# Kernel tuning notes

Measured on AMD Instinct MI355X. Metric: run time of the kernel, lower is better.

## Reference

```python
import jax, jax.numpy as jnp
import numpy as np

D_MODEL = 1024
H = 16
D_K = D_MODEL // H  # 64
B, S = 2, 2048


def setup_inputs() -> dict:
    key = jax.random.key(0)
    ks = jax.random.split(key, 8)
    scale = 1.0 / np.sqrt(D_MODEL)
    return {
        "q": jax.random.normal(ks[0], (B, S, D_MODEL), dtype=jnp.float32),
        "k": jax.random.normal(ks[1], (B, S, D_MODEL), dtype=jnp.float32),
        "v": jax.random.normal(ks[2], (B, S, D_MODEL), dtype=jnp.float32),
        "W_q": jax.random.normal(ks[3], (H, D_MODEL, D_K), dtype=jnp.float32) * scale,
        "W_k": jax.random.normal(ks[4], (H, D_MODEL, D_K), dtype=jnp.float32) * scale,
        "W_v": jax.random.normal(ks[5], (H, D_MODEL, D_K), dtype=jnp.float32) * scale,
        "W_o": jax.random.normal(ks[6], (D_MODEL, H * D_K), dtype=jnp.float32) * scale,
        "b_o": jnp.zeros((D_MODEL,), dtype=jnp.float32),
    }


def reference(q, k, v, W_q, W_k, W_v, W_o, b_o):
    b, s, _ = q.shape
    h, _, d_k = W_q.shape
    inv_sqrt_dk = jnp.asarray(1.0 / np.sqrt(d_k), q.dtype)
    # per-head projections: [b, h, s, d_k]
    qh = jnp.einsum("bsd,hdk->bhsk", q, W_q)
    kh = jnp.einsum("bsd,hdk->bhsk", k, W_k)
    vh = jnp.einsum("bsd,hdk->bhsk", v, W_v)
    # scaled dot product attention
    scores = jnp.einsum("bhqk,bhsk->bhqs", qh, kh) * inv_sqrt_dk  # [b,h,S,S]
    attn = jax.nn.softmax(scores, axis=-1)
    ctx = jnp.einsum("bhqs,bhsk->bhqk", attn, vh)  # [b,h,S,d_k]
    # chunk over heads + concat along feature dim -> [b, S, h*d_k], head-major
    ctx = ctx.transpose(0, 2, 1, 3).reshape(b, s, h * d_k)
    # final linear
    return ctx @ W_o.T + b_o
```

## Files before the change

### kernel.cpp

```cpp
#include <hip/hip_runtime.h>
#include <cstdint>
#include <cstddef>


typedef unsigned short bf16_t;
typedef __attribute__((ext_vector_type(8))) short short8;
typedef __attribute__((ext_vector_type(4))) float f32x4;

#define GLB_AS(p) ((const __attribute__((address_space(1))) void*)(p))
#define LDS_AS(p) ((__attribute__((address_space(3))) void*)(p))

__device__ __forceinline__ uint32_t fbits(float f) {
  union { float f; uint32_t u; } v; v.f = f; return v.u;
}
__device__ __forceinline__ bf16_t f2bf(float f) {
  uint32_t u = fbits(f);
  return (bf16_t)((u + 0x7FFFu + ((u >> 16) & 1u)) >> 16);
}
__device__ __forceinline__ uint32_t packbf2(float lo, float hi) {
  uint32_t a = fbits(hi) + 0x8000u;
  uint32_t b = fbits(lo) + 0x8000u;
  return __builtin_amdgcn_perm(a, b, 0x07060302u);
}

__global__ void prep_kernel(const float* __restrict__ q, const float* __restrict__ k,
                            const float* __restrict__ v, const float* __restrict__ Wo,
                            const float* __restrict__ Wq, const float* __restrict__ Wk,
                            const float* __restrict__ Wv,
                            bf16_t* __restrict__ qo, bf16_t* __restrict__ ko,
                            bf16_t* __restrict__ vo, bf16_t* __restrict__ Woo,
                            bf16_t* __restrict__ Wtq, bf16_t* __restrict__ Wtk,
                            bf16_t* __restrict__ Wtv) {
  int blk = blockIdx.x;
  int tid = threadIdx.x;
  if (blk < 13312) {
    const float* src; bf16_t* dst; int i;
    if (blk < 4096)       { src = q;  dst = qo;  i = blk * 256 + tid; }
    else if (blk < 8192)  { src = k;  dst = ko;  i = (blk - 4096) * 256 + tid; }
    else if (blk < 12288) { src = v;  dst = vo;  i = (blk - 8192) * 256 + tid; }
    else                  { src = Wo; dst = Woo; i = (blk - 12288) * 256 + tid; }
    f32x4 val = ((const f32x4*)src)[i];
    ushort4 o;
    o.x = f2bf(val.x); o.y = f2bf(val.y); o.z = f2bf(val.z); o.w = f2bf(val.w);
    ((ushort4*)dst)[i] = o;
  } else {
    int blk2 = blk - 13312;
    int z = blk2 >> 9, t = blk2 & 511;
    const float* W = z == 0 ? Wq : z == 1 ? Wk : Wv;
    bf16_t* Wt = z == 0 ? Wtq : z == 1 ? Wtk : Wtv;
    int h = t >> 5, d0 = (t & 31) * 32;
    __shared__ float tile[32][65];
    const float* src = W + ((size_t)h << 16) + (size_t)d0 * 64;
    int d = tid >> 3;
#pragma unroll
    for (int j = 0; j < 2; j++) {
      int dk = (tid & 7) * 8 + j * 4;
      *(f32x4*)&tile[d][dk] = *(const f32x4*)(src + d * 64 + dk);
    }
    __syncthreads();
    int dk2 = tid >> 2, c = tid & 3;
    union { ushort s[8]; int4 v; } o;
#pragma unroll
    for (int j = 0; j < 8; j++) o.s[j] = f2bf(tile[c * 8 + j][dk2]);
    *(int4*)(Wt + (size_t)(h * 64 + dk2) * 1024 + d0 + c * 8) = o.v;
  }
}

__global__ void v_transpose_kernel(const bf16_t* __restrict__ vh, bf16_t* __restrict__ vT) {
  __shared__ bf16_t tile[64][72];
  const int tid = threadIdx.x;
  const int s0 = blockIdx.x * 64;
  const size_t bh = blockIdx.y;
  const bf16_t* src = vh + bh * (2048 * 64) + (size_t)s0 * 64;
#pragma unroll
  for (int j = 0; j < 2; j++) {
    int cidx = tid + j * 256, s = cidx >> 3, ck = cidx & 7;
    *(int4*)(&tile[s][ck * 8]) = *(const int4*)(src + s * 64 + ck * 8);
  }
  __syncthreads();
  bf16_t* dst = vT + bh * (64 * 2048) + s0;
#pragma unroll
  for (int j = 0; j < 2; j++) {
    int cidx = tid + j * 256, dk = cidx >> 3, cs = cidx & 7;
    union { ushort s[8]; int4 v; } o;
#pragma unroll
    for (int e = 0; e < 8; e++) o.s[e] = tile[cs * 8 + e][dk];
    *(int4*)(dst + (size_t)dk * 2048 + cs * 8) = o.v;
  }
}

__global__ __launch_bounds__(256) void gemm_proj_kernel(
    const bf16_t* __restrict__ A0, const bf16_t* __restrict__ A1, const bf16_t* __restrict__ A2,
    const bf16_t* __restrict__ B0, const bf16_t* __restrict__ B1, const bf16_t* __restrict__ B2,
    bf16_t* __restrict__ O0, bf16_t* __restrict__ O1, bf16_t* __restrict__ O2,
    float s0)
{
  const int z = blockIdx.z;
  const bf16_t* A  = z == 0 ? A0 : z == 1 ? A1 : A2;
  const bf16_t* Bt = z == 0 ? B0 : z == 1 ? B1 : B2;
  bf16_t* Cbf      = z == 0 ? O0 : z == 1 ? O1 : O2;
  const float scale = z == 0 ? s0 : 1.0f;
  const int K = 1024;

  __shared__ alignas(16) bf16_t Asmem[128 * 32];
  __shared__ alignas(16) bf16_t Bsmem[128 * 32];
  const int tid = threadIdx.x;
  const int lane = tid & 63, wave = tid >> 6;
  const int wm = wave >> 1, wn = wave & 1;
  const int quad = lane >> 4, l15 = lane & 15;
  const int m0 = blockIdx.y * 128, n0 = blockIdx.x * 128;

  f32x4 acc[4][4];
#pragma unroll
  for (int i = 0; i < 4; i++)
#pragma unroll
    for (int j = 0; j < 4; j++) acc[i][j] = (f32x4)0.0f;

  const int c0 = wave * 128 + lane;
  const int c1 = wave * 128 + 64 + lane;

  for (int k0 = 0; k0 < K; k0 += 32) {
    __builtin_amdgcn_global_load_lds(GLB_AS(A  + (size_t)(m0 + (c0 >> 2)) * K + k0 + (c0 & 3) * 8),
                                     LDS_AS(Asmem + c0 * 8), 16, 0, 0);
    __builtin_amdgcn_global_load_lds(GLB_AS(A  + (size_t)(m0 + (c1 >> 2)) * K + k0 + (c1 & 3) * 8),
                                     LDS_AS(Asmem + c1 * 8), 16, 0, 0);
    __builtin_amdgcn_global_load_lds(GLB_AS(Bt + (size_t)(n0 + (c0 >> 2)) * K + k0 + (c0 & 3) * 8),
                                     LDS_AS(Bsmem + c0 * 8), 16, 0, 0);
    __builtin_amdgcn_global_load_lds(GLB_AS(Bt + (size_t)(n0 + (c1 >> 2)) * K + k0 + (c1 & 3) * 8),
                                     LDS_AS(Bsmem + c1 * 8), 16, 0, 0);
    __syncthreads();

    short8 af[4], bfr[4];
#pragma unroll
    for (int mi = 0; mi < 4; mi++)
      af[mi] = *(const short8*)(Asmem + (wm * 64 + mi * 16 + l15) * 32 + quad * 8);
#pragma unroll
    for (int ni = 0; ni < 4; ni++)
      bfr[ni] = *(const short8*)(Bsmem + (wn * 64 + ni * 16 + l15) * 32 + quad * 8);
#pragma unroll
    for (int mi = 0; mi < 4; mi++)
#pragma unroll
      for (int ni = 0; ni < 4; ni++)
        acc[mi][ni] = __builtin_amdgcn_mfma_f32_16x16x32_bf16(af[mi], bfr[ni], acc[mi][ni], 0, 0, 0);
    __syncthreads();
  }

#pragma unroll
  for (int ni = 0; ni < 4; ni++) {
    int col = n0 + wn * 64 + ni * 16 + l15;
    int h = col >> 6, dk = col & 63;
#pragma unroll
    for (int mi = 0; mi < 4; mi++) {
      int row = m0 + wm * 64 + mi * 16 + quad * 4;
#pragma unroll
      for (int r = 0; r < 4; r++) {
        int g = row + r;
        int b = g >> 11, s = g & 2047;
        Cbf[((size_t)((b * 16 + h) * 2048 + s)) * 64 + dk] = f2bf(acc[mi][ni][r] * scale);
      }
    }
  }
}

__global__ __launch_bounds__(256) void gemm_out_kernel(
    const bf16_t* __restrict__ A, const bf16_t* __restrict__ Bt,
    float* __restrict__ C, const float* __restrict__ bias)
{
  const int K = 1024, N = 1024;
  __shared__ alignas(16) bf16_t Asmem[128 * 32];
  __shared__ alignas(16) bf16_t Bsmem[64 * 32];
  const int tid = threadIdx.x;
  const int lane = tid & 63, wave = tid >> 6;
  const int quad = lane >> 4, l15 = lane & 15;
  const int m0 = blockIdx.y * 128, n0 = blockIdx.x * 64;

  f32x4 acc[2][4];
#pragma unroll
  for (int i = 0; i < 2; i++)
#pragma unroll
    for (int j = 0; j < 4; j++) acc[i][j] = (f32x4)0.0f;

  const int c0 = wave * 128 + lane;
  const int c1 = wave * 128 + 64 + lane;
  const int cb = wave * 64 + lane;

  for (int k0 = 0; k0 < K; k0 += 32) {
    __builtin_amdgcn_global_load_lds(GLB_AS(A  + (size_t)(m0 + (c0 >> 2)) * K + k0 + (c0 & 3) * 8),
                                     LDS_AS(Asmem + c0 * 8), 16, 0, 0);
    __builtin_amdgcn_global_load_lds(GLB_AS(A  + (size_t)(m0 + (c1 >> 2)) * K + k0 + (c1 & 3) * 8),
                                     LDS_AS(Asmem + c1 * 8), 16, 0, 0);
    __builtin_amdgcn_global_load_lds(GLB_AS(Bt + (size_t)(n0 + (cb >> 2)) * K + k0 + (cb & 3) * 8),
                                     LDS_AS(Bsmem + cb * 8), 16, 0, 0);
    __syncthreads();

    short8 af[2], bfr[4];
#pragma unroll
    for (int mi = 0; mi < 2; mi++)
      af[mi] = *(const short8*)(Asmem + (wave * 32 + mi * 16 + l15) * 32 + quad * 8);
#pragma unroll
    for (int ni = 0; ni < 4; ni++)
      bfr[ni] = *(const short8*)(Bsmem + (ni * 16 + l15) * 32 + quad * 8);
#pragma unroll
    for (int mi = 0; mi < 2; mi++)
#pragma unroll
      for (int ni = 0; ni < 4; ni++)
        acc[mi][ni] = __builtin_amdgcn_mfma_f32_16x16x32_bf16(af[mi], bfr[ni], acc[mi][ni], 0, 0, 0);
    __syncthreads();
  }

#pragma unroll
  for (int ni = 0; ni < 4; ni++) {
    int col = n0 + ni * 16 + l15;
    float bv = bias[col];
#pragma unroll
    for (int mi = 0; mi < 2; mi++) {
      int row = m0 + wave * 32 + mi * 16 + quad * 4;
#pragma unroll
      for (int r = 0; r < 4; r++)
        C[(size_t)(row + r) * N + col] = acc[mi][ni][r] + bv;
    }
  }
}

__global__ __launch_bounds__(512) void flash_kernel(
    const bf16_t* __restrict__ qh, const bf16_t* __restrict__ kh,
    const bf16_t* __restrict__ vT, bf16_t* __restrict__ ctx)
{
  __shared__ alignas(16) bf16_t Kt[2][64 * 72];
  __shared__ alignas(16) bf16_t Vt[2][64 * 72];
  __shared__ alignas(16) bf16_t Pt[8][16 * 72];
  const int tid = threadIdx.x, lane = tid & 63, wave = tid >> 6;
  const int quad = lane >> 4, l15 = lane & 15;
  const int q0 = blockIdx.x * 128;
  const int h = blockIdx.y, b = blockIdx.z;
  const size_t headoff = (size_t)(b * 16 + h) * 2048 * 64;
  const bf16_t* Q = qh + headoff;
  const bf16_t* K = kh + headoff;
  const bf16_t* V = vT + headoff;
  bf16_t* Ptw = &Pt[wave][0];

  const int qrow = q0 + wave * 16 + l15;
  short8 qf[2];
#pragma unroll
  for (int ks = 0; ks < 2; ks++)
    qf[ks] = *(const short8*)(Q + (size_t)qrow * 64 + ks * 32 + quad * 8);

  f32x4 O[4];
#pragma unroll
  for (int mi = 0; mi < 4; mi++) O[mi] = (f32x4)0.0f;
  f32x4 lacc = (f32x4)0.0f;

  const int sr = tid >> 3, scc = tid & 7;
  const bf16_t* Kp = K + (size_t)sr * 64 + scc * 8;
  const bf16_t* Vp = V + (size_t)sr * 2048 + scc * 8;
  const int soff = sr * 72 + scc * 8;

  int4 kreg = *(const int4*)Kp;
  int4 vreg = *(const int4*)Vp;
  *(int4*)(&Kt[0][soff]) = kreg;
  *(int4*)(&Vt[0][soff]) = vreg;
  __syncthreads();

  for (int it = 0; it < 32; ++it) {
    const int cur = it & 1, nxt = cur ^ 1;
    if (it < 31) {
      kreg = *(const int4*)(Kp + (size_t)(it + 1) * 64 * 64);
      vreg = *(const int4*)(Vp + (it + 1) * 64);
    }

    f32x4 S[4];
#pragma unroll
    for (int mi = 0; mi < 4; mi++) S[mi] = (f32x4)0.0f;
#pragma unroll
    for (int ks = 0; ks < 2; ks++) {
#pragma unroll
      for (int mi = 0; mi < 4; mi++) {
        short8 kf = *(const short8*)(&Kt[cur][(mi * 16 + l15) * 72 + ks * 32 + quad * 8]);
        S[mi] = __builtin_amdgcn_mfma_f32_16x16x32_bf16(kf, qf[ks], S[mi], 0, 0, 0);
      }
    }

#pragma unroll
    for (int mi = 0; mi < 4; mi++)
#pragma unroll
      for (int r = 0; r < 4; r++)
        S[mi][r] = __builtin_amdgcn_exp2f(S[mi][r]);
    lacc += (S[0] + S[1]) + (S[2] + S[3]);

#pragma unroll
    for (int mi = 0; mi < 4; mi++) {
      uint2 pk = make_uint2(packbf2(S[mi][0], S[mi][1]), packbf2(S[mi][2], S[mi][3]));
      *(uint2*)(Ptw + l15 * 72 + mi * 16 + quad * 4) = pk;
    }

#pragma unroll
    for (int ks = 0; ks < 2; ks++) {
      short8 pfrag = *(const short8*)(Ptw + l15 * 72 + ks * 32 + quad * 8);
#pragma unroll
      for (int mi = 0; mi < 4; mi++) {
        short8 vf = *(const short8*)(&Vt[cur][(mi * 16 + l15) * 72 + ks * 32 + quad * 8]);
        O[mi] = __builtin_amdgcn_mfma_f32_16x16x32_bf16(vf, pfrag, O[mi], 0, 0, 0);
      }
    }

    if (it < 31) {
      *(int4*)(&Kt[nxt][soff]) = kreg;
      *(int4*)(&Vt[nxt][soff]) = vreg;
    }
    __syncthreads();
  }

  float l = (lacc[0] + lacc[1]) + (lacc[2] + lacc[3]);
  l += __shfl_xor(l, 16, 64);
  l += __shfl_xor(l, 32, 64);
  float inv = 1.0f / l;
  bf16_t* crow = ctx + ((size_t)(b * 2048 + qrow)) * 1024 + h * 64;
#pragma unroll
  for (int mi = 0; mi < 4; mi++) {
    uint2 pk = make_uint2(packbf2(O[mi][0] * inv, O[mi][1] * inv),
                          packbf2(O[mi][2] * inv, O[mi][3] * inv));
    *(uint2*)(crow + mi * 16 + quad * 4) = pk;
  }
}

extern "C" void kernel_launch(void* const* d_in, const int* in_sizes, int n_in,
                              void* d_out, int out_size, void* d_ws, size_t ws_size,
                              hipStream_t stream)
{
  const float* q  = (const float*)d_in[0];
  const float* k  = (const float*)d_in[1];
  const float* v  = (const float*)d_in[2];
  const float* Wq = (const float*)d_in[3];
  const float* Wk = (const float*)d_in[4];
  const float* Wv = (const float*)d_in[5];
  const float* Wo = (const float*)d_in[6];
  const float* bo = (const float*)d_in[7];
  float* out = (float*)d_out;

  const size_t NX = (size_t)4096 * 1024;
  const size_t NW = (size_t)1024 * 1024;

  char* p = (char*)d_ws;
  bf16_t* qbf = (bf16_t*)p; p += NX * 2;
  bf16_t* kbf = (bf16_t*)p; p += NX * 2;
  bf16_t* vbf = (bf16_t*)p; p += NX * 2;
  bf16_t* Wtq = (bf16_t*)p; p += NW * 2;
  bf16_t* Wtk = (bf16_t*)p; p += NW * 2;
  bf16_t* Wtv = (bf16_t*)p; p += NW * 2;
  bf16_t* Wob = (bf16_t*)p; p += NW * 2;
  bf16_t* qhb = (bf16_t*)p; p += NX * 2;
  bf16_t* khb = (bf16_t*)p; p += NX * 2;
  bf16_t* vhb = (bf16_t*)p; p += NX * 2;
  bf16_t* vTb = (bf16_t*)p; p += NX * 2;
  bf16_t* ctxb = (bf16_t*)p; p += NX * 2;

  prep_kernel<<<14848, 256, 0, stream>>>(q, k, v, Wo, Wq, Wk, Wv,
                                         qbf, kbf, vbf, Wob, Wtq, Wtk, Wtv);

  const float qscale = 0.125f * 1.44269504088896340736f;
  gemm_proj_kernel<<<dim3(8, 32, 3), 256, 0, stream>>>(qbf, kbf, vbf, Wtq, Wtk, Wtv,
                                                       qhb, khb, vhb, qscale);

  v_transpose_kernel<<<dim3(32, 32), 256, 0, stream>>>(vhb, vTb);

  flash_kernel<<<dim3(16, 16, 2), 512, 0, stream>>>(qhb, khb, vTb, ctxb);

  gemm_out_kernel<<<dim3(16, 32), 256, 0, stream>>>(ctxb, Wob, out, bo);

  (void)in_sizes; (void)n_in; (void)out_size; (void)ws_size;
}
```

Baseline: 228.5 us.

## Fuse V transpose into projection GEMM epilogue and use fragment-ordered LDS in flash

The projection GEMM epilogue now stages results through shared memory and writes coalesced 16-byte stores. For V it writes the transposed layout directly, which removes the separate v_transpose kernel and its global round trip. The flash kernel stores K, V and P tiles in LDS in MFMA fragment order, so each lane reads contiguous 16 bytes without padding, aiming to reduce bank conflicts. The cost is extra barriers and LDS traffic in the GEMM epilogue.

```diff
diff --git a/kernel.cpp b/kernel.cpp
--- a/kernel.cpp
+++ b/kernel.cpp
@@ -66,29 +66,6 @@
   }
 }
 
-__global__ void v_transpose_kernel(const bf16_t* __restrict__ vh, bf16_t* __restrict__ vT) {
-  __shared__ bf16_t tile[64][72];
-  const int tid = threadIdx.x;
-  const int s0 = blockIdx.x * 64;
-  const size_t bh = blockIdx.y;
-  const bf16_t* src = vh + bh * (2048 * 64) + (size_t)s0 * 64;
-#pragma unroll
-  for (int j = 0; j < 2; j++) {
-    int cidx = tid + j * 256, s = cidx >> 3, ck = cidx & 7;
-    *(int4*)(&tile[s][ck * 8]) = *(const int4*)(src + s * 64 + ck * 8);
-  }
-  __syncthreads();
-  bf16_t* dst = vT + bh * (64 * 2048) + s0;
-#pragma unroll
-  for (int j = 0; j < 2; j++) {
-    int cidx = tid + j * 256, dk = cidx >> 3, cs = cidx & 7;
-    union { ushort s[8]; int4 v; } o;
-#pragma unroll
-    for (int e = 0; e < 8; e++) o.s[e] = tile[cs * 8 + e][dk];
-    *(int4*)(dst + (size_t)dk * 2048 + cs * 8) = o.v;
-  }
-}
-
 __global__ __launch_bounds__(256) void gemm_proj_kernel(
     const bf16_t* __restrict__ A0, const bf16_t* __restrict__ A1, const bf16_t* __restrict__ A2,
     const bf16_t* __restrict__ B0, const bf16_t* __restrict__ B1, const bf16_t* __restrict__ B2,
@@ -98,12 +75,14 @@
   const int z = blockIdx.z;
   const bf16_t* A  = z == 0 ? A0 : z == 1 ? A1 : A2;
   const bf16_t* Bt = z == 0 ? B0 : z == 1 ? B1 : B2;
-  bf16_t* Cbf      = z == 0 ? O0 : z == 1 ? O1 : O2;
+  bf16_t* Cout     = z == 0 ? O0 : z == 1 ? O1 : O2;
   const float scale = z == 0 ? s0 : 1.0f;
   const int K = 1024;
 
-  __shared__ alignas(16) bf16_t Asmem[128 * 32];
-  __shared__ alignas(16) bf16_t Bsmem[128 * 32];
+  __shared__ alignas(16) bf16_t smem[128 * 72];
+  bf16_t* Asmem = smem;
+  bf16_t* Bsmem = smem + 128 * 32;
+
   const int tid = threadIdx.x;
   const int lane = tid & 63, wave = tid >> 6;
   const int wm = wave >> 1, wn = wave & 1;
@@ -145,19 +124,56 @@
     __syncthreads();
   }
 
-#pragma unroll
-  for (int ni = 0; ni < 4; ni++) {
-    int col = n0 + wn * 64 + ni * 16 + l15;
-    int h = col >> 6, dk = col & 63;
-#pragma unroll
-    for (int mi = 0; mi < 4; mi++) {
-      int row = m0 + wm * 64 + mi * 16 + quad * 4;
-#pragma unroll
-      for (int r = 0; r < 4; r++) {
-        int g = row + r;
-        int b = g >> 11, s = g & 2047;
-        Cbf[((size_t)((b * 16 + h) * 2048 + s)) * 64 + dk] = f2bf(acc[mi][ni][r] * scale);
-      }
+  const int s0r = m0 & 2047, bb = m0 >> 11;
+  if (z < 2) {
+#pragma unroll
+    for (int p = 0; p < 2; p++) {
+      if (wn == p) {
+#pragma unroll
+        for (int ni = 0; ni < 4; ni++)
+#pragma unroll
+          for (int mi = 0; mi < 4; mi++)
+#pragma unroll
+            for (int r = 0; r < 4; r++)
+              smem[(wm * 64 + mi * 16 + quad * 4 + r) * 72 + ni * 16 + l15] =
+                  f2bf(acc[mi][ni][r] * scale);
+      }
+      __syncthreads();
+      int hp = (n0 >> 6) + p;
+      bf16_t* dstbase = Cout + (((size_t)(bb * 16 + hp)) * 2048 + s0r) * 64;
+#pragma unroll
+      for (int rd = 0; rd < 4; rd++) {
+        int idx = rd * 256 + tid;
+        int m = idx >> 3, c8 = idx & 7;
+        int4 val = *(const int4*)(smem + m * 72 + c8 * 8);
+        *(int4*)(dstbase + (size_t)m * 64 + c8 * 8) = val;
+      }
+      __syncthreads();
+    }
+  } else {
+#pragma unroll
+    for (int p = 0; p < 2; p++) {
+      if (wn == p) {
+#pragma unroll
+        for (int ni = 0; ni < 4; ni++)
+#pragma unroll
+          for (int mi = 0; mi < 4; mi++) {
+            uint2 pk = make_uint2(packbf2(acc[mi][ni][0], acc[mi][ni][1]),
+                                  packbf2(acc[mi][ni][2], acc[mi][ni][3]));
+            *(uint2*)(smem + (ni * 16 + l15) * 136 + wm * 64 + mi * 16 + quad * 4) = pk;
+          }
+      }
+      __syncthreads();
+      int hp = (n0 >> 6) + p;
+      bf16_t* dstbase = Cout + ((size_t)(bb * 16 + hp)) * 64 * 2048 + s0r;
+#pragma unroll
+      for (int rd = 0; rd < 4; rd++) {
+        int idx = rd * 256 + tid;
+        int c = idx >> 4, ck = idx & 15;
+        int4 val = *(const int4*)(smem + c * 136 + ck * 8);
+        *(int4*)(dstbase + (size_t)c * 2048 + ck * 8) = val;
+      }
+      __syncthreads();
     }
   }
 }
@@ -226,9 +242,9 @@
     const bf16_t* __restrict__ qh, const bf16_t* __restrict__ kh,
     const bf16_t* __restrict__ vT, bf16_t* __restrict__ ctx)
 {
-  __shared__ alignas(16) bf16_t Kt[2][64 * 72];
-  __shared__ alignas(16) bf16_t Vt[2][64 * 72];
-  __shared__ alignas(16) bf16_t Pt[8][16 * 72];
+  __shared__ alignas(16) bf16_t KtF[2][4096];
+  __shared__ alignas(16) bf16_t VtF[2][4096];
+  __shared__ alignas(16) bf16_t PtF[8 * 1024];
   const int tid = threadIdx.x, lane = tid & 63, wave = tid >> 6;
   const int quad = lane >> 4, l15 = lane & 15;
   const int q0 = blockIdx.x * 128;
@@ -237,7 +253,6 @@
   const bf16_t* Q = qh + headoff;
   const bf16_t* K = kh + headoff;
   const bf16_t* V = vT + headoff;
-  bf16_t* Ptw = &Pt[wave][0];
 
   const int qrow = q0 + wave * 16 + l15;
   short8 qf[2];
@@ -250,21 +265,22 @@
   for (int mi = 0; mi < 4; mi++) O[mi] = (f32x4)0.0f;
   f32x4 lacc = (f32x4)0.0f;
 
-  const int sr = tid >> 3, scc = tid & 7;
-  const bf16_t* Kp = K + (size_t)sr * 64 + scc * 8;
-  const bf16_t* Vp = V + (size_t)sr * 2048 + scc * 8;
-  const int soff = sr * 72 + scc * 8;
+  const bf16_t* Kp = K + (size_t)((wave >> 1) * 16 + l15) * 64 + (wave & 1) * 32 + quad * 8;
+  const bf16_t* Vp = V + (size_t)((wave >> 1) * 16 + l15) * 2048 + (wave & 1) * 32 + quad * 8;
+  const int soff = wave * 512 + lane * 8;
+
+  const int pwbase = wave * 2048 + ((quad >> 1) * 16 + l15) * 16 + 8 * (quad & 1);
 
   int4 kreg = *(const int4*)Kp;
   int4 vreg = *(const int4*)Vp;
-  *(int4*)(&Kt[0][soff]) = kreg;
-  *(int4*)(&Vt[0][soff]) = vreg;
+  *(int4*)(&KtF[0][soff]) = kreg;
+  *(int4*)(&VtF[0][soff]) = vreg;
   __syncthreads();
 
   for (int it = 0; it < 32; ++it) {
     const int cur = it & 1, nxt = cur ^ 1;
     if (it < 31) {
-      kreg = *(const int4*)(Kp + (size_t)(it + 1) * 64 * 64);
+      kreg = *(const int4*)(Kp + (size_t)(it + 1) * 4096);
       vreg = *(const int4*)(Vp + (it + 1) * 64);
     }
 
@@ -275,7 +291,7 @@
     for (int ks = 0; ks < 2; ks++) {
 #pragma unroll
       for (int mi = 0; mi < 4; mi++) {
-        short8 kf = *(const short8*)(&Kt[cur][(mi * 16 + l15) * 72 + ks * 32 + quad * 8]);
+        short8 kf = *(const short8*)(&KtF[cur][(mi * 2 + ks) * 512 + lane * 8]);
         S[mi] = __builtin_amdgcn_mfma_f32_16x16x32_bf16(kf, qf[ks], S[mi], 0, 0, 0);
       }
     }
@@ -290,22 +306,22 @@
 #pragma unroll
     for (int mi = 0; mi < 4; mi++) {
       uint2 pk = make_uint2(packbf2(S[mi][0], S[mi][1]), packbf2(S[mi][2], S[mi][3]));
-      *(uint2*)(Ptw + l15 * 72 + mi * 16 + quad * 4) = pk;
+      *(uint2*)((char*)PtF + pwbase + (mi >> 1) * 1024 + (mi & 1) * 512) = pk;
     }
 
 #pragma unroll
     for (int ks = 0; ks < 2; ks++) {
-      short8 pfrag = *(const short8*)(Ptw + l15 * 72 + ks * 32 + quad * 8);
+      short8 pfrag = *(const short8*)(&PtF[wave * 1024 + (ks * 64 + lane) * 8]);
 #pragma unroll
       for (int mi = 0; mi < 4; mi++) {
-        short8 vf = *(const short8*)(&Vt[cur][(mi * 16 + l15) * 72 + ks * 32 + quad * 8]);
+        short8 vf = *(const short8*)(&VtF[cur][(mi * 2 + ks) * 512 + lane * 8]);
         O[mi] = __builtin_amdgcn_mfma_f32_16x16x32_bf16(vf, pfrag, O[mi], 0, 0, 0);
       }
     }
 
     if (it < 31) {
-      *(int4*)(&Kt[nxt][soff]) = kreg;
-      *(int4*)(&Vt[nxt][soff]) = vreg;
+      *(int4*)(&KtF[nxt][soff]) = kreg;
+      *(int4*)(&VtF[nxt][soff]) = vreg;
     }
     __syncthreads();
   }
@@ -350,7 +366,6 @@
   bf16_t* Wob = (bf16_t*)p; p += NW * 2;
   bf16_t* qhb = (bf16_t*)p; p += NX * 2;
   bf16_t* khb = (bf16_t*)p; p += NX * 2;
-  bf16_t* vhb = (bf16_t*)p; p += NX * 2;
   bf16_t* vTb = (bf16_t*)p; p += NX * 2;
   bf16_t* ctxb = (bf16_t*)p; p += NX * 2;
 
@@ -359,9 +374,7 @@
 
   const float qscale = 0.125f * 1.44269504088896340736f;
   gemm_proj_kernel<<<dim3(8, 32, 3), 256, 0, stream>>>(qbf, kbf, vbf, Wtq, Wtk, Wtv,
-                                                       qhb, khb, vhb, qscale);
-
-  v_transpose_kernel<<<dim3(32, 32), 256, 0, stream>>>(vhb, vTb);
+                                                       qhb, khb, vTb, qscale);
 
   flash_kernel<<<dim3(16, 16, 2), 512, 0, stream>>>(qhb, khb, vTb, ctxb);
 
```

Result: no change. 231.0 us (+1.1%).
